# Kernel tuning notes

Measured on AMD Instinct MI355X. Metric: run time of the kernel, lower is better.

## Reference

```python
import jax, jax.numpy as jnp
import numpy as np

# FrictionConfig constants (chosen in init_kwargs)
K_STEPS = 4
ETA = 0.1
ETA_DECAY = 0.9
MU_MAX = 10.0
SMOOTH_LAMBDA = 0.1
RADIUS = 8
B, S, H = 4, 2048, 1024
INNER = max(H // 2, 32)  # 512


def _build_window_edges(length, radius):
    chunks = []
    for d in range(1, radius + 1):
        i = np.arange(length - d, dtype=np.int32)
        chunks.append(np.stack([i, i + d], axis=1))
    return np.concatenate(chunks, axis=0)  # [E, 2]


def setup_inputs() -> dict:
    key = jax.random.key(0)
    ks = jax.random.split(key, 8)
    hidden = jax.random.normal(ks[0], (B, S, H), dtype=jnp.float32)
    attention_mask = jnp.ones((B, S), dtype=jnp.int32)
    edges = jnp.asarray(_build_window_edges(S, RADIUS))
    # edge_mlp: Linear(2, INNER) -> GELU -> Linear(INNER, 1)
    W1 = jax.random.normal(ks[1], (2, INNER), dtype=jnp.float32) * (1.0 / np.sqrt(2))
    b1 = jnp.zeros((INNER,), dtype=jnp.float32)
    W2 = jax.random.normal(ks[2], (INNER, 1), dtype=jnp.float32) * (1.0 / np.sqrt(INNER))
    b2 = jnp.zeros((1,), dtype=jnp.float32)
    # q_proj: Linear(H, H)
    Wq = jax.random.normal(ks[3], (H, H), dtype=jnp.float32) * (1.0 / np.sqrt(H))
    bq = jnp.zeros((H,), dtype=jnp.float32)
    # LayerNorm
    gamma = jnp.ones((H,), dtype=jnp.float32)
    beta = jnp.zeros((H,), dtype=jnp.float32)
    return {"hidden": hidden, "attention_mask": attention_mask, "edges": edges,
            "Wq": Wq, "bq": bq, "W1": W1, "b1": b1, "W2": W2, "b2": b2,
            "gamma": gamma, "beta": beta}


def _edge_weights(h, ei, ej, W1, b1, W2, b2):
    hi = h[ei]  # [E, H]
    hj = h[ej]
    diff = hi - hj
    dist = jnp.linalg.norm(diff, axis=-1, keepdims=True)           # [E, 1]
    ni = jnp.maximum(jnp.linalg.norm(hi, axis=-1), 1e-6)
    nj = jnp.maximum(jnp.linalg.norm(hj, axis=-1), 1e-6)
    cos = (jnp.sum(hi * hj, axis=-1) / (ni * nj))[:, None]         # [E, 1]
    feats = jnp.concatenate([dist, cos], axis=-1)                  # [E, 2]
    z = jax.nn.gelu(feats @ W1 + b1, approximate=False) @ W2 + b2  # [E, 1]
    return jax.nn.softplus(z) + 1e-5


def _laplacian(h, ei, ej, mu):
    n = h.shape[0]
    weighted = mu * (h[ei] - h[ej])  # [E, H]
    # normalize_laplacian = True
    w = mu[:, 0]
    deg = jnp.zeros((n,), h.dtype).at[ei].add(w).at[ej].add(w)
    inv_sqrt = jnp.maximum(deg, 1e-6) ** -0.5
    weighted = weighted * (inv_sqrt[ei] * inv_sqrt[ej])[:, None]
    lap = jnp.zeros_like(h).at[ei].add(weighted).at[ej].add(-weighted)
    return lap


def _smooth(s):
    left = jnp.concatenate([s[:1], s[:-1]], axis=0)
    right = jnp.concatenate([s[1:], s[-1:]], axis=0)
    return s - SMOOTH_LAMBDA * (2.0 * s - left - right)


def _layernorm(x, gamma, beta):
    m = x.mean(axis=-1, keepdims=True)
    v = x.var(axis=-1, keepdims=True)
    return (x - m) * jax.lax.rsqrt(v + 1e-5) * gamma + beta


def _run_single(h, ei, ej, Wq, bq, W1, b1, W2, b2, gamma, beta):
    q = h @ Wq + bq
    state = h
    mu = None
    for step in range(K_STEPS):
        mu = _edge_weights(state, ei, ej, W1, b1, W2, b2)  # recompute_mu=True
        mu = jnp.minimum(mu, MU_MAX)
        lap = _laplacian(state, ei, ej, mu)
        eta = ETA * (ETA_DECAY ** step)
        state = state - eta * (lap - q)
        state = _smooth(state)
    out = _layernorm(state + h, gamma, beta)
    diffs = state[ei] - state[ej]
    energy = 0.5 * jnp.sum(mu[:, 0] * jnp.sum(diffs * diffs, axis=-1))
    return out, energy


def reference(hidden, attention_mask, edges, Wq, bq, W1, b1, W2, b2, gamma, beta):
    # All masks are full-length, so edges are identical across batch and
    # the outer Python batch loop vectorizes to a vmap.
    ei, ej = edges[:, 0], edges[:, 1]
    outputs, energy = jax.vmap(
        lambda h: _run_single(h, ei, ej, Wq, bq, W1, b1, W2, b2, gamma, beta)
    )(hidden)
    return outputs, energy
```

## Files before the change

### kernel.cpp

```cpp
#include <hip/hip_runtime.h>

#define BB 4
#define SS 2048
#define HH 1024
#define TG 8
#define TU 32
#define CW 256

typedef unsigned short u16;
typedef __bf16 bf16x8 __attribute__((ext_vector_type(8)));
typedef float f32x4 __attribute__((ext_vector_type(4)));

__device__ __forceinline__ float b2f(u16 u){
  union { unsigned int i; float f; } v; v.i = ((unsigned int)u) << 16; return v.f;
}
__device__ __forceinline__ u16 f2b(float f){
  union { float f; unsigned int i; } v; v.f = f;
  unsigned int x = v.i;
  return (u16)((x + 0x7fffu + ((x >> 16) & 1u)) >> 16);
}
__device__ __forceinline__ float4 u4f(ushort4 v){
  float4 o; o.x = b2f(v.x); o.y = b2f(v.y); o.z = b2f(v.z); o.w = b2f(v.w); return o;
}
__device__ __forceinline__ ushort4 f4u(float4 v){
  ushort4 o; o.x = f2b(v.x); o.y = f2b(v.y); o.z = f2b(v.z); o.w = f2b(v.w); return o;
}
__device__ __forceinline__ float wave_sum(float v){
  #pragma unroll
  for(int m = 32; m > 0; m >>= 1) v += __shfl_xor(v, m);
  return v;
}
__device__ __forceinline__ float pread(const void* p, int i, int f){
  return f ? b2f(((const u16*)p)[i]) : ((const float*)p)[i];
}
__device__ __forceinline__ void gload16(const void* g, void* l){
  __builtin_amdgcn_global_load_lds((const __attribute__((address_space(1))) unsigned int*)g,
                                   (__attribute__((address_space(3))) unsigned int*)l, 16, 0, 0);
}
__device__ __forceinline__ float fast_gelu(float z){
  float x  = z * 0.70710678118654752f;
  float ax = fabsf(x);
  float t  = __builtin_amdgcn_rcpf(fmaf(0.3275911f, ax, 1.f));
  float poly = ((((1.061405429f*t - 1.453152027f)*t + 1.421413741f)*t
                 - 0.284496736f)*t + 0.254829592f)*t;
  float er = fmaf(-poly, __expf(-ax*ax), 1.f);
  er = (x < 0.f) ? -er : er;
  return 0.5f*z*(1.f + er);
}

__global__ __launch_bounds__(256) void k_params(const void* bq, const void* W1, const void* b1,
                                                const void* W2, const void* b2, const void* gm,
                                                const void* bt, float* bqc, float* W1c, float* b1c,
                                                float* W2c, float* b2c, float* gmc, float* btc,
                                                int* flagp){
  __shared__ int sf;
  if(threadIdx.x == 0){
    int f = (((const u16*)gm)[0] == 0x3F80u) ? 1 : 0;
    sf = f; *flagp = f;
  }
  __syncthreads();
  int f = sf, t = threadIdx.x;
  for(int i = t; i < 1024; i += 256) bqc[i] = pread(bq, i, f);
  for(int i = t; i < 1024; i += 256) W1c[i] = pread(W1, i, f);
  for(int i = t; i <  512; i += 256) b1c[i] = pread(b1, i, f);
  for(int i = t; i <  512; i += 256) W2c[i] = pread(W2, i, f);
  if(t == 0) b2c[0] = pread(b2, 0, f);
  for(int i = t; i < 1024; i += 256) gmc[i] = pread(gm, i, f);
  for(int i = t; i < 1024; i += 256) btc[i] = pread(bt, i, f);
}

__global__ __launch_bounds__(256) void k_cvt(const void* h, u16* s, const int* flagp){
  int f = *flagp;
  size_t i4 = (size_t)blockIdx.x*256 + threadIdx.x;
  if(f){
    ((ushort4*)s)[i4] = ((const ushort4*)h)[i4];
  } else {
    float4 v = ((const float4*)h)[i4];
    ((ushort4*)s)[i4] = f4u(v);
  }
}

__global__ __launch_bounds__(256) void k_transpose(const void* W, u16* __restrict__ Wt,
                                                   const int* flagp){
  int f = *flagp;
  __shared__ u16 t[32][33];
  int bx = blockIdx.x, by = blockIdx.y;
  int tx = threadIdx.x, ty = threadIdx.y;
  #pragma unroll
  for(int r = 0; r < 32; r += 8){
    int idx = (by*32 + ty + r)*HH + bx*32 + tx;
    float v = f ? b2f(((const u16*)W)[idx]) : ((const float*)W)[idx];
    t[ty + r][tx] = f2b(v);
  }
  __syncthreads();
  #pragma unroll
  for(int r = 0; r < 32; r += 8)
    Wt[(size_t)(bx*32 + ty + r)*HH + by*32 + tx] = t[tx][ty + r];
}

__global__ __launch_bounds__(256) void k_qgemm(const u16* __restrict__ A, const u16* __restrict__ Wt,
                                               const float* __restrict__ bqc, u16* __restrict__ q){
  __shared__ u16 lA[128*32];
  __shared__ u16 lB[128*32];
  int m0 = blockIdx.x*128, n0 = blockIdx.y*128;
  int tid  = threadIdx.x;
  int wave = tid >> 6, lane = tid & 63;
  int wm = (wave >> 1)*64, wn = (wave & 1)*64;
  int quad = lane >> 4, l16 = lane & 15;
  int srow = tid >> 2;
  int scol = (tid & 3)*8;

  f32x4 acc[4][4];
  #pragma unroll
  for(int i = 0; i < 4; i++)
    #pragma unroll
    for(int j = 0; j < 4; j++) acc[i][j] = (f32x4){0.f,0.f,0.f,0.f};

  for(int k0 = 0; k0 < HH; k0 += 32){
    __syncthreads();
    gload16(A  + (size_t)(m0 + srow     )*HH + k0 + scol, &lA[ srow     *32 + scol]);
    gload16(A  + (size_t)(m0 + srow + 64)*HH + k0 + scol, &lA[(srow+64) *32 + scol]);
    gload16(Wt + (size_t)(n0 + srow     )*HH + k0 + scol, &lB[ srow     *32 + scol]);
    gload16(Wt + (size_t)(n0 + srow + 64)*HH + k0 + scol, &lB[(srow+64) *32 + scol]);
    __syncthreads();
    bf16x8 af[4];
    #pragma unroll
    for(int mt = 0; mt < 4; mt++)
      af[mt] = *(const bf16x8*)&lA[(wm + mt*16 + l16)*32 + quad*8];
    #pragma unroll
    for(int nt = 0; nt < 4; nt++){
      bf16x8 bf = *(const bf16x8*)&lB[(wn + nt*16 + l16)*32 + quad*8];
      #pragma unroll
      for(int mt = 0; mt < 4; mt++)
        acc[mt][nt] = __builtin_amdgcn_mfma_f32_16x16x32_bf16(af[mt], bf, acc[mt][nt], 0, 0, 0);
    }
  }
  #pragma unroll
  for(int nt = 0; nt < 4; nt++){
    int col = n0 + wn + nt*16 + l16;
    float bqv = bqc[col];
    #pragma unroll
    for(int mt = 0; mt < 4; mt++){
      #pragma unroll
      for(int r = 0; r < 4; r++){
        int row = m0 + wm + mt*16 + quad*4 + r;
        q[(size_t)row*HH + col] = f2b(acc[mt][nt][r] + bqv);
      }
    }
  }
}

__global__ __launch_bounds__(128) void k_gram_mu(const u16* __restrict__ s,
                                                 const float* __restrict__ W1c, const float* __restrict__ b1c,
                                                 const float* __restrict__ W2c, const float* __restrict__ b2c,
                                                 float* __restrict__ mu){
  __shared__ float Gband[16*9];
  __shared__ float4 wpk[512];
  int b = blockIdx.y, i0 = blockIdx.x*TG;
  int tid = threadIdx.x, wave = tid >> 6, lane = tid & 63;

  #pragma unroll
  for(int i = tid; i < 512; i += 128)
    wpk[i] = make_float4(W1c[i], W1c[512+i], b1c[i], W2c[i]);

  if(wave == 0){
    int quad = lane >> 4, l16 = lane & 15;
    int ra = i0 + l16; if(ra > SS-1) ra = SS-1;
    const u16* ar = s + ((size_t)b*SS + ra)*HH + quad*8;
    f32x4 acc = (f32x4){0.f,0.f,0.f,0.f};
    #pragma unroll 8
    for(int k0 = 0; k0 < HH; k0 += 32){
      bf16x8 af = *(const bf16x8*)(ar + k0);
      acc = __builtin_amdgcn_mfma_f32_16x16x32_bf16(af, af, acc, 0, 0, 0);
    }
    #pragma unroll
    for(int r = 0; r < 4; r++){
      int gr = quad*4 + r;
      int dd = l16 - gr;
      if(dd >= 0 && dd <= 8) Gband[gr*9 + dd] = acc[r];
    }
  }
  __syncthreads();

  int e = tid >> 1, h = tid & 1;
  int d = (e >> 3) + 1, k = e & 7;
  bool valid = (i0 + k + d) < SS;
  float gii = Gband[k*9], gjj = Gband[(k+d)*9], gij = Gband[k*9 + d];
  float dist = sqrtf(fmaxf(gii + gjj - 2.f*gij, 0.f));
  float ni = fmaxf(sqrtf(gii), 1e-6f);
  float nj = fmaxf(sqrtf(gjj), 1e-6f);
  float cosv = gij * __builtin_amdgcn_rcpf(ni * nj);
  float acc = 0.f;
  const float4* wp = &wpk[h*256];
  #pragma unroll 4
  for(int j0 = 0; j0 < 256; j0++){
    float4 wv = wp[j0];
    float z1 = fmaf(dist, wv.x, fmaf(cosv, wv.y, wv.z));
    acc = fmaf(fast_gelu(z1), wv.w, acc);
  }
  acc += __shfl_xor(acc, 1);
  if(h == 0 && valid){
    float z  = acc + b2c[0];
    float sp = fmaxf(z, 0.f) + __logf(1.f + __expf(-fabsf(z)));
    mu[((size_t)b*8 + (d-1))*SS + (i0 + k)] = fminf(sp + 1e-5f, 10.0f);
  }
}

__global__ __launch_bounds__(256) void k_upsm(const u16* __restrict__ sIn, u16* __restrict__ sOut,
                                              const u16* __restrict__ q, const float* __restrict__ mu,
                                              float eta){
  __shared__ u16 st[50*CW];
  __shared__ u16 up[34*CW];
  __shared__ float invsS[50];
  __shared__ float muS[58*8];
  int i0 = blockIdx.x*TU, c0 = blockIdx.y*CW, b = blockIdx.z;
  int tid = threadIdx.x;

  for(int idx = tid; idx < 58*8; idx += 256){
    int ir = idx >> 3, d = (idx & 7) + 1;
    int i = i0 - 17 + ir;
    float v = 0.f;
    if(i >= 0 && i + d < SS) v = mu[((size_t)b*8 + d-1)*SS + i];
    muS[idx] = v;
  }
  for(int idx = tid; idx < 50*(CW/4); idx += 256){
    int r = idx / (CW/4), cc = idx % (CW/4);
    int i = i0 - 9 + r;
    ushort4 v = {0,0,0,0};
    if(i >= 0 && i < SS) v = *(const ushort4*)(sIn + ((size_t)b*SS + i)*HH + c0 + cc*4);
    ((ushort4*)st)[idx] = v;
  }
  __syncthreads();
  if(tid < 50){
    int ir = tid + 8;
    float deg = 0.f;
    #pragma unroll
    for(int d = 1; d <= 8; d++){
      deg += muS[ir*8 + d-1];
      deg += muS[(ir-d)*8 + d-1];
    }
    invsS[tid] = 1.0f / sqrtf(fmaxf(deg, 1e-6f));
  }
  __syncthreads();

  int rq = tid >> 6, lane = tid & 63;
  for(int jr = 0; jr < 9; jr++){
    int r = rq + jr*4;
    if(r >= 34) break;
    int i = i0 - 1 + r;
    if(i < 0 || i >= SS) continue;
    int sr = r + 8, vr = r + 8, mr = r + 16;
    float inv_i = invsS[vr];
    float4 si = u4f(((const ushort4*)(st + (size_t)sr*CW))[lane]);
    float A = 0.f;
    float4 acc = {0.f,0.f,0.f,0.f};
    #pragma unroll
    for(int d = 1; d <= 8; d++){
      float cR = muS[mr*8 + d-1]     * inv_i        * invsS[vr+d];
      float cL = muS[(mr-d)*8 + d-1] * invsS[vr-d]  * inv_i;
      A += cR + cL;
      float4 vR = u4f(((const ushort4*)(st + (size_t)(sr+d)*CW))[lane]);
      float4 vL = u4f(((const ushort4*)(st + (size_t)(sr-d)*CW))[lane]);
      acc.x -= cR*vR.x + cL*vL.x; acc.y -= cR*vR.y + cL*vL.y;
      acc.z -= cR*vR.z + cL*vL.z; acc.w -= cR*vR.w + cL*vL.w;
    }
    acc.x += A*si.x; acc.y += A*si.y; acc.z += A*si.z; acc.w += A*si.w;
    float4 qv = u4f(*(const ushort4*)(q + ((size_t)b*SS + i)*HH + c0 + lane*4));
    float4 o;
    o.x = si.x - eta*(acc.x - qv.x);
    o.y = si.y - eta*(acc.y - qv.y);
    o.z = si.z - eta*(acc.z - qv.z);
    o.w = si.w - eta*(acc.w - qv.w);
    ((ushort4*)(up + (size_t)r*CW))[lane] = f4u(o);
  }
  __syncthreads();
  for(int js = 0; js < 8; js++){
    int rr = rq + js*4;
    int i = i0 + rr;
    int ur = rr + 1;
    float4 c  = u4f(((const ushort4*)(up + (size_t)ur*CW))[lane]);
    float4 l  = (i > 0)      ? u4f(((const ushort4*)(up + (size_t)(ur-1)*CW))[lane]) : c;
    float4 r4 = (i < SS-1)   ? u4f(((const ushort4*)(up + (size_t)(ur+1)*CW))[lane]) : c;
    float4 o;
    o.x = c.x - 0.1f*(2.f*c.x - l.x - r4.x);
    o.y = c.y - 0.1f*(2.f*c.y - l.y - r4.y);
    o.z = c.z - 0.1f*(2.f*c.z - l.z - r4.z);
    o.w = c.w - 0.1f*(2.f*c.w - l.w - r4.w);
    *(ushort4*)(sOut + ((size_t)b*SS + i)*HH + c0 + lane*4) = f4u(o);
  }
}

__global__ __launch_bounds__(256) void k_out(const u16* __restrict__ sA, const void* __restrict__ hraw,
                                             const float* __restrict__ gmc, const float* __restrict__ btc,
                                             void* __restrict__ outp, const int* flagp){
  int f = *flagp;
  int b = blockIdx.x >> 11, i = blockIdx.x & (SS-1);
  int tid = threadIdx.x;
  size_t row = (size_t)b*SS + i;
  float4 sv = u4f(((const ushort4*)(sA + row*HH))[tid]);
  float4 hv;
  if(f) hv = u4f(((const ushort4*)((const u16*)hraw + row*HH))[tid]);
  else  hv = ((const float4*)((const float*)hraw + row*HH))[tid];
  float x0 = sv.x + hv.x, x1 = sv.y + hv.y, x2 = sv.z + hv.z, x3 = sv.w + hv.w;

  __shared__ float sh[4];
  int wv = tid >> 6, lane = tid & 63;
  float lsum = wave_sum(x0 + x1 + x2 + x3);
  if(lane == 0) sh[wv] = lsum;
  __syncthreads();
  float mean = (sh[0] + sh[1] + sh[2] + sh[3]) * (1.f/HH);
  __syncthreads();
  float d0 = x0-mean, d1 = x1-mean, d2 = x2-mean, d3 = x3-mean;
  float lsq = wave_sum(d0*d0 + d1*d1 + d2*d2 + d3*d3);
  if(lane == 0) sh[wv] = lsq;
  __syncthreads();
  float var = (sh[0] + sh[1] + sh[2] + sh[3]) * (1.f/HH);
  float sc = 1.0f / sqrtf(var + 1e-5f);

  int col = tid*4;
  float4 o;
  o.x = d0*sc*gmc[col+0] + btc[col+0];
  o.y = d1*sc*gmc[col+1] + btc[col+1];
  o.z = d2*sc*gmc[col+2] + btc[col+2];
  o.w = d3*sc*gmc[col+3] + btc[col+3];
  if(f) ((ushort4*)((u16*)outp + row*HH))[tid] = f4u(o);
  else  ((float4*)((float*)outp + row*HH))[tid] = o;
}

__global__ __launch_bounds__(128) void k_energy(const u16* __restrict__ s, const float* __restrict__ mu,
                                                float* __restrict__ partials){
  __shared__ float Gband[16*9];
  int b = blockIdx.y, i0 = blockIdx.x*TG;
  int tid = threadIdx.x, wave = tid >> 6, lane = tid & 63;

  if(wave == 0){
    int quad = lane >> 4, l16 = lane & 15;
    int ra = i0 + l16; if(ra > SS-1) ra = SS-1;
    const u16* ar = s + ((size_t)b*SS + ra)*HH + quad*8;
    f32x4 acc = (f32x4){0.f,0.f,0.f,0.f};
    #pragma unroll 8
    for(int k0 = 0; k0 < HH; k0 += 32){
      bf16x8 af = *(const bf16x8*)(ar + k0);
      acc = __builtin_amdgcn_mfma_f32_16x16x32_bf16(af, af, acc, 0, 0, 0);
    }
    #pragma unroll
    for(int r = 0; r < 4; r++){
      int gr = quad*4 + r;
      int dd = l16 - gr;
      if(dd >= 0 && dd <= 8) Gband[gr*9 + dd] = acc[r];
    }
  }
  __syncthreads();
  if(wave == 0){
    int d = (lane >> 3) + 1, k = lane & 7;
    float esum = 0.f;
    if((i0 + k + d) < SS){
      float d2 = fmaxf(Gband[k*9] + Gband[(k+d)*9] - 2.f*Gband[k*9 + d], 0.f);
      esum = mu[((size_t)b*8 + (d-1))*SS + (i0 + k)] * d2;
    }
    esum = wave_sum(esum);
    if(lane == 0) partials[(size_t)b*256 + blockIdx.x] = esum;
  }
}

__global__ __launch_bounds__(256) void k_efinal(const float* __restrict__ partials, void* __restrict__ outp,
                                                const int* flagp){
  int f = *flagp;
  int b = blockIdx.x;
  float sacc = partials[(size_t)b*256 + threadIdx.x];
  sacc = wave_sum(sacc);
  __shared__ float sh[4];
  if((threadIdx.x & 63) == 0) sh[threadIdx.x >> 6] = sacc;
  __syncthreads();
  if(threadIdx.x == 0){
    float e = 0.5f * (sh[0] + sh[1] + sh[2] + sh[3]);
    if(f) ((u16*)outp)[(size_t)BB*SS*HH + b] = f2b(e);
    else  ((float*)outp)[(size_t)BB*SS*HH + b] = e;
  }
}

extern "C" void kernel_launch(void* const* d_in, const int* in_sizes, int n_in,
                              void* d_out, int out_size, void* d_ws, size_t ws_size,
                              hipStream_t stream) {
  const void* hidden = d_in[0];
  const void* Wq  = d_in[3];
  const void* bq  = d_in[4];
  const void* W1  = d_in[5];
  const void* b1  = d_in[6];
  const void* W2  = d_in[7];
  const void* b2v = d_in[8];
  const void* gamma = d_in[9];
  const void* beta  = d_in[10];

  char* w = (char*)d_ws;
  u16*   q   = (u16*)w;   w += (size_t)BB*SS*HH*2;
  u16*   sA  = (u16*)w;   w += (size_t)BB*SS*HH*2;
  u16*   Wt  = (u16*)w;   w += (size_t)HH*HH*2;
  float* mu  = (float*)w; w += (size_t)BB*8*SS*4;
  float* partials = (float*)w; w += (size_t)BB*256*4;
  float* bqc = (float*)w; w += 1024*4;
  float* W1c = (float*)w; w += 1024*4;
  float* b1c = (float*)w; w += 512*4;
  float* W2c = (float*)w; w += 512*4;
  float* b2c = (float*)w; w += 4;
  float* gmc = (float*)w; w += 1024*4;
  float* btc = (float*)w; w += 1024*4;
  int*   flagp = (int*)w; w += 4;
  u16* sB = (u16*)d_out;

  k_params   <<<1, 256, 0, stream>>>(bq, W1, b1, W2, b2v, gamma, beta,
                                     bqc, W1c, b1c, W2c, b2c, gmc, btc, flagp);
  k_cvt      <<<(BB*SS*HH/4)/256, 256, 0, stream>>>(hidden, sA, flagp);
  k_transpose<<<dim3(HH/32, HH/32), dim3(32,8), 0, stream>>>(Wq, Wt, flagp);
  k_qgemm    <<<dim3(BB*SS/128, HH/128), 256, 0, stream>>>(sA, Wt, bqc, q);

  const float etas[4] = {0.1f, 0.09f, 0.081f, 0.0729f};
  for(int step = 0; step < 4; step++){
    const u16* cur = (step & 1) ? sB : sA;
    u16*       nxt = (step & 1) ? sA : sB;
    k_gram_mu<<<dim3(SS/TG, BB), 128, 0, stream>>>(cur, W1c, b1c, W2c, b2c, mu);
    k_upsm   <<<dim3(SS/TU, HH/CW, BB), 256, 0, stream>>>(cur, nxt, q, mu, etas[step]);
  }
  k_out   <<<BB*SS, 256, 0, stream>>>(sA, hidden, gmc, btc, d_out, flagp);
  k_energy<<<dim3(SS/TG, BB), 128, 0, stream>>>(sA, mu, partials);
  k_efinal<<<BB, 256, 0, stream>>>(partials, d_out, flagp);
}
```

Baseline: 415.8 us.

## Fuse all stages into one persistent megakernel with grid-wide barriers

Replaces the sequence of separate launches (param convert, cast, transpose, q GEMM, per-step gram/mu and update/smooth kernels, layernorm, energy) with a single persistent kernel that loops over work units and uses a software grid barrier between phases. The gram computation is also split across all four waves with partial Gram reductions in shared memory, and the MLP loop is split four ways per edge. This is meant to remove launch overhead and idle tails between the many small kernels. In exchange it relies on all blocks being co-resident (grid sized from occupancy queries), adds atomic spin-barrier cost, and may lose per-kernel tuning such as occupancy for the GEMM phase.

Result: slower. 977.9 us (+135.2%).

```diff
diff --git a/kernel.cpp b/kernel.cpp
--- a/kernel.cpp
+++ b/kernel.cpp
@@ -3,13 +3,32 @@
 #define BB 4
 #define SS 2048
 #define HH 1024
-#define TG 8
 #define TU 32
 #define CW 256
+#define MAXG 768
 
 typedef unsigned short u16;
 typedef __bf16 bf16x8 __attribute__((ext_vector_type(8)));
 typedef float f32x4 __attribute__((ext_vector_type(4)));
+
+#define SMEM_BYTES 45072
+#define OFF_ST    0
+#define OFF_UP    25600
+#define OFF_MUS   43008
+#define OFF_INV   44864
+#define OFF_WPK   0
+#define OFF_GPART 8192
+#define OFF_GBAND 10496
+#define OFF_LA    0
+#define OFF_LB    8192
+
+#define QBYTES   ((size_t)BB*SS*HH*2)
+#define WS_Q     ((size_t)0)
+#define WS_SA    QBYTES
+#define WS_WT    (2*QBYTES)
+#define WS_MU    (2*QBYTES + (size_t)HH*HH*2)
+#define WS_PART  (WS_MU + (size_t)BB*8*SS*4)
+#define WS_PAR   (WS_PART + 4096)
 
 __device__ __forceinline__ float b2f(u16 u){
   union { unsigned int i; float f; } v; v.i = ((unsigned int)u) << 16; return v.f;
@@ -48,380 +67,390 @@
   return 0.5f*z*(1.f + er);
 }
 
-__global__ __launch_bounds__(256) void k_params(const void* bq, const void* W1, const void* b1,
-                                                const void* W2, const void* b2, const void* gm,
-                                                const void* bt, float* bqc, float* W1c, float* b1c,
-                                                float* W2c, float* b2c, float* gmc, float* btc,
-                                                int* flagp){
-  __shared__ int sf;
-  if(threadIdx.x == 0){
-    int f = (((const u16*)gm)[0] == 0x3F80u) ? 1 : 0;
-    sf = f; *flagp = f;
-  }
-  __syncthreads();
-  int f = sf, t = threadIdx.x;
-  for(int i = t; i < 1024; i += 256) bqc[i] = pread(bq, i, f);
-  for(int i = t; i < 1024; i += 256) W1c[i] = pread(W1, i, f);
-  for(int i = t; i <  512; i += 256) b1c[i] = pread(b1, i, f);
-  for(int i = t; i <  512; i += 256) W2c[i] = pread(W2, i, f);
-  if(t == 0) b2c[0] = pread(b2, 0, f);
-  for(int i = t; i < 1024; i += 256) gmc[i] = pread(gm, i, f);
-  for(int i = t; i < 1024; i += 256) btc[i] = pread(bt, i, f);
-}
-
-__global__ __launch_bounds__(256) void k_cvt(const void* h, u16* s, const int* flagp){
-  int f = *flagp;
-  size_t i4 = (size_t)blockIdx.x*256 + threadIdx.x;
-  if(f){
-    ((ushort4*)s)[i4] = ((const ushort4*)h)[i4];
-  } else {
-    float4 v = ((const float4*)h)[i4];
-    ((ushort4*)s)[i4] = f4u(v);
-  }
-}
-
-__global__ __launch_bounds__(256) void k_transpose(const void* W, u16* __restrict__ Wt,
-                                                   const int* flagp){
-  int f = *flagp;
-  __shared__ u16 t[32][33];
-  int bx = blockIdx.x, by = blockIdx.y;
-  int tx = threadIdx.x, ty = threadIdx.y;
-  #pragma unroll
-  for(int r = 0; r < 32; r += 8){
-    int idx = (by*32 + ty + r)*HH + bx*32 + tx;
-    float v = f ? b2f(((const u16*)W)[idx]) : ((const float*)W)[idx];
-    t[ty + r][tx] = f2b(v);
-  }
-  __syncthreads();
-  #pragma unroll
-  for(int r = 0; r < 32; r += 8)
-    Wt[(size_t)(bx*32 + ty + r)*HH + by*32 + tx] = t[tx][ty + r];
-}
-
-__global__ __launch_bounds__(256) void k_qgemm(const u16* __restrict__ A, const u16* __restrict__ Wt,
-                                               const float* __restrict__ bqc, u16* __restrict__ q){
-  __shared__ u16 lA[128*32];
-  __shared__ u16 lB[128*32];
-  int m0 = blockIdx.x*128, n0 = blockIdx.y*128;
-  int tid  = threadIdx.x;
-  int wave = tid >> 6, lane = tid & 63;
-  int wm = (wave >> 1)*64, wn = (wave & 1)*64;
-  int quad = lane >> 4, l16 = lane & 15;
-  int srow = tid >> 2;
-  int scol = (tid & 3)*8;
-
-  f32x4 acc[4][4];
-  #pragma unroll
-  for(int i = 0; i < 4; i++)
-    #pragma unroll
-    for(int j = 0; j < 4; j++) acc[i][j] = (f32x4){0.f,0.f,0.f,0.f};
-
-  for(int k0 = 0; k0 < HH; k0 += 32){
-    __syncthreads();
-    gload16(A  + (size_t)(m0 + srow     )*HH + k0 + scol, &lA[ srow     *32 + scol]);
-    gload16(A  + (size_t)(m0 + srow + 64)*HH + k0 + scol, &lA[(srow+64) *32 + scol]);
-    gload16(Wt + (size_t)(n0 + srow     )*HH + k0 + scol, &lB[ srow     *32 + scol]);
-    gload16(Wt + (size_t)(n0 + srow + 64)*HH + k0 + scol, &lB[(srow+64) *32 + scol]);
-    __syncthreads();
-    bf16x8 af[4];
-    #pragma unroll
-    for(int mt = 0; mt < 4; mt++)
-      af[mt] = *(const bf16x8*)&lA[(wm + mt*16 + l16)*32 + quad*8];
-    #pragma unroll
-    for(int nt = 0; nt < 4; nt++){
-      bf16x8 bf = *(const bf16x8*)&lB[(wn + nt*16 + l16)*32 + quad*8];
-      #pragma unroll
-      for(int mt = 0; mt < 4; mt++)
-        acc[mt][nt] = __builtin_amdgcn_mfma_f32_16x16x32_bf16(af[mt], bf, acc[mt][nt], 0, 0, 0);
-    }
-  }
-  #pragma unroll
-  for(int nt = 0; nt < 4; nt++){
-    int col = n0 + wn + nt*16 + l16;
-    float bqv = bqc[col];
-    #pragma unroll
-    for(int mt = 0; mt < 4; mt++){
-      #pragma unroll
-      for(int r = 0; r < 4; r++){
-        int row = m0 + wm + mt*16 + quad*4 + r;
-        q[(size_t)row*HH + col] = f2b(acc[mt][nt][r] + bqv);
-      }
-    }
-  }
-}
-
-__global__ __launch_bounds__(128) void k_gram_mu(const u16* __restrict__ s,
-                                                 const float* __restrict__ W1c, const float* __restrict__ b1c,
-                                                 const float* __restrict__ W2c, const float* __restrict__ b2c,
-                                                 float* __restrict__ mu){
-  __shared__ float Gband[16*9];
-  __shared__ float4 wpk[512];
-  int b = blockIdx.y, i0 = blockIdx.x*TG;
-  int tid = threadIdx.x, wave = tid >> 6, lane = tid & 63;
-
-  #pragma unroll
-  for(int i = tid; i < 512; i += 128)
-    wpk[i] = make_float4(W1c[i], W1c[512+i], b1c[i], W2c[i]);
-
-  if(wave == 0){
-    int quad = lane >> 4, l16 = lane & 15;
-    int ra = i0 + l16; if(ra > SS-1) ra = SS-1;
-    const u16* ar = s + ((size_t)b*SS + ra)*HH + quad*8;
-    f32x4 acc = (f32x4){0.f,0.f,0.f,0.f};
-    #pragma unroll 8
-    for(int k0 = 0; k0 < HH; k0 += 32){
-      bf16x8 af = *(const bf16x8*)(ar + k0);
-      acc = __builtin_amdgcn_mfma_f32_16x16x32_bf16(af, af, acc, 0, 0, 0);
-    }
-    #pragma unroll
-    for(int r = 0; r < 4; r++){
-      int gr = quad*4 + r;
-      int dd = l16 - gr;
-      if(dd >= 0 && dd <= 8) Gband[gr*9 + dd] = acc[r];
-    }
-  }
-  __syncthreads();
-
-  int e = tid >> 1, h = tid & 1;
-  int d = (e >> 3) + 1, k = e & 7;
-  bool valid = (i0 + k + d) < SS;
-  float gii = Gband[k*9], gjj = Gband[(k+d)*9], gij = Gband[k*9 + d];
-  float dist = sqrtf(fmaxf(gii + gjj - 2.f*gij, 0.f));
-  float ni = fmaxf(sqrtf(gii), 1e-6f);
-  float nj = fmaxf(sqrtf(gjj), 1e-6f);
-  float cosv = gij * __builtin_amdgcn_rcpf(ni * nj);
-  float acc = 0.f;
-  const float4* wp = &wpk[h*256];
-  #pragma unroll 4
-  for(int j0 = 0; j0 < 256; j0++){
-    float4 wv = wp[j0];
-    float z1 = fmaf(dist, wv.x, fmaf(cosv, wv.y, wv.z));
-    acc = fmaf(fast_gelu(z1), wv.w, acc);
-  }
-  acc += __shfl_xor(acc, 1);
-  if(h == 0 && valid){
-    float z  = acc + b2c[0];
-    float sp = fmaxf(z, 0.f) + __logf(1.f + __expf(-fabsf(z)));
-    mu[((size_t)b*8 + (d-1))*SS + (i0 + k)] = fminf(sp + 1e-5f, 10.0f);
-  }
-}
-
-__global__ __launch_bounds__(256) void k_upsm(const u16* __restrict__ sIn, u16* __restrict__ sOut,
-                                              const u16* __restrict__ q, const float* __restrict__ mu,
-                                              float eta){
-  __shared__ u16 st[50*CW];
-  __shared__ u16 up[34*CW];
-  __shared__ float invsS[50];
-  __shared__ float muS[58*8];
-  int i0 = blockIdx.x*TU, c0 = blockIdx.y*CW, b = blockIdx.z;
-  int tid = threadIdx.x;
-
-  for(int idx = tid; idx < 58*8; idx += 256){
-    int ir = idx >> 3, d = (idx & 7) + 1;
-    int i = i0 - 17 + ir;
-    float v = 0.f;
-    if(i >= 0 && i + d < SS) v = mu[((size_t)b*8 + d-1)*SS + i];
-    muS[idx] = v;
-  }
-  for(int idx = tid; idx < 50*(CW/4); idx += 256){
-    int r = idx / (CW/4), cc = idx % (CW/4);
-    int i = i0 - 9 + r;
-    ushort4 v = {0,0,0,0};
-    if(i >= 0 && i < SS) v = *(const ushort4*)(sIn + ((size_t)b*SS + i)*HH + c0 + cc*4);
-    ((ushort4*)st)[idx] = v;
-  }
-  __syncthreads();
-  if(tid < 50){
-    int ir = tid + 8;
-    float deg = 0.f;
-    #pragma unroll
-    for(int d = 1; d <= 8; d++){
-      deg += muS[ir*8 + d-1];
-      deg += muS[(ir-d)*8 + d-1];
-    }
-    invsS[tid] = 1.0f / sqrtf(fmaxf(deg, 1e-6f));
-  }
-  __syncthreads();
-
-  int rq = tid >> 6, lane = tid & 63;
-  for(int jr = 0; jr < 9; jr++){
-    int r = rq + jr*4;
-    if(r >= 34) break;
-    int i = i0 - 1 + r;
-    if(i < 0 || i >= SS) continue;
-    int sr = r + 8, vr = r + 8, mr = r + 16;
-    float inv_i = invsS[vr];
-    float4 si = u4f(((const ushort4*)(st + (size_t)sr*CW))[lane]);
-    float A = 0.f;
-    float4 acc = {0.f,0.f,0.f,0.f};
-    #pragma unroll
-    for(int d = 1; d <= 8; d++){
-      float cR = muS[mr*8 + d-1]     * inv_i        * invsS[vr+d];
-      float cL = muS[(mr-d)*8 + d-1] * invsS[vr-d]  * inv_i;
-      A += cR + cL;
-      float4 vR = u4f(((const ushort4*)(st + (size_t)(sr+d)*CW))[lane]);
-      float4 vL = u4f(((const ushort4*)(st + (size_t)(sr-d)*CW))[lane]);
-      acc.x -= cR*vR.x + cL*vL.x; acc.y -= cR*vR.y + cL*vL.y;
-      acc.z -= cR*vR.z + cL*vL.z; acc.w -= cR*vR.w + cL*vL.w;
-    }
-    acc.x += A*si.x; acc.y += A*si.y; acc.z += A*si.z; acc.w += A*si.w;
-    float4 qv = u4f(*(const ushort4*)(q + ((size_t)b*SS + i)*HH + c0 + lane*4));
-    float4 o;
-    o.x = si.x - eta*(acc.x - qv.x);
-    o.y = si.y - eta*(acc.y - qv.y);
-    o.z = si.z - eta*(acc.z - qv.z);
-    o.w = si.w - eta*(acc.w - qv.w);
-    ((ushort4*)(up + (size_t)r*CW))[lane] = f4u(o);
-  }
-  __syncthreads();
-  for(int js = 0; js < 8; js++){
-    int rr = rq + js*4;
-    int i = i0 + rr;
-    int ur = rr + 1;
-    float4 c  = u4f(((const ushort4*)(up + (size_t)ur*CW))[lane]);
-    float4 l  = (i > 0)      ? u4f(((const ushort4*)(up + (size_t)(ur-1)*CW))[lane]) : c;
-    float4 r4 = (i < SS-1)   ? u4f(((const ushort4*)(up + (size_t)(ur+1)*CW))[lane]) : c;
-    float4 o;
-    o.x = c.x - 0.1f*(2.f*c.x - l.x - r4.x);
-    o.y = c.y - 0.1f*(2.f*c.y - l.y - r4.y);
-    o.z = c.z - 0.1f*(2.f*c.z - l.z - r4.z);
-    o.w = c.w - 0.1f*(2.f*c.w - l.w - r4.w);
-    *(ushort4*)(sOut + ((size_t)b*SS + i)*HH + c0 + lane*4) = f4u(o);
-  }
-}
-
-__global__ __launch_bounds__(256) void k_out(const u16* __restrict__ sA, const void* __restrict__ hraw,
-                                             const float* __restrict__ gmc, const float* __restrict__ btc,
-                                             void* __restrict__ outp, const int* flagp){
-  int f = *flagp;
-  int b = blockIdx.x >> 11, i = blockIdx.x & (SS-1);
-  int tid = threadIdx.x;
-  size_t row = (size_t)b*SS + i;
-  float4 sv = u4f(((const ushort4*)(sA + row*HH))[tid]);
-  float4 hv;
-  if(f) hv = u4f(((const ushort4*)((const u16*)hraw + row*HH))[tid]);
-  else  hv = ((const float4*)((const float*)hraw + row*HH))[tid];
-  float x0 = sv.x + hv.x, x1 = sv.y + hv.y, x2 = sv.z + hv.z, x3 = sv.w + hv.w;
-
-  __shared__ float sh[4];
-  int wv = tid >> 6, lane = tid & 63;
-  float lsum = wave_sum(x0 + x1 + x2 + x3);
-  if(lane == 0) sh[wv] = lsum;
-  __syncthreads();
-  float mean = (sh[0] + sh[1] + sh[2] + sh[3]) * (1.f/HH);
-  __syncthreads();
-  float d0 = x0-mean, d1 = x1-mean, d2 = x2-mean, d3 = x3-mean;
-  float lsq = wave_sum(d0*d0 + d1*d1 + d2*d2 + d3*d3);
-  if(lane == 0) sh[wv] = lsq;
-  __syncthreads();
-  float var = (sh[0] + sh[1] + sh[2] + sh[3]) * (1.f/HH);
-  float sc = 1.0f / sqrtf(var + 1e-5f);
-
-  int col = tid*4;
-  float4 o;
-  o.x = d0*sc*gmc[col+0] + btc[col+0];
-  o.y = d1*sc*gmc[col+1] + btc[col+1];
-  o.z = d2*sc*gmc[col+2] + btc[col+2];
-  o.w = d3*sc*gmc[col+3] + btc[col+3];
-  if(f) ((ushort4*)((u16*)outp + row*HH))[tid] = f4u(o);
-  else  ((float4*)((float*)outp + row*HH))[tid] = o;
-}
-
-__global__ __launch_bounds__(128) void k_energy(const u16* __restrict__ s, const float* __restrict__ mu,
-                                                float* __restrict__ partials){
-  __shared__ float Gband[16*9];
-  int b = blockIdx.y, i0 = blockIdx.x*TG;
-  int tid = threadIdx.x, wave = tid >> 6, lane = tid & 63;
-
-  if(wave == 0){
-    int quad = lane >> 4, l16 = lane & 15;
-    int ra = i0 + l16; if(ra > SS-1) ra = SS-1;
-    const u16* ar = s + ((size_t)b*SS + ra)*HH + quad*8;
-    f32x4 acc = (f32x4){0.f,0.f,0.f,0.f};
-    #pragma unroll 8
-    for(int k0 = 0; k0 < HH; k0 += 32){
-      bf16x8 af = *(const bf16x8*)(ar + k0);
-      acc = __builtin_amdgcn_mfma_f32_16x16x32_bf16(af, af, acc, 0, 0, 0);
-    }
-    #pragma unroll
-    for(int r = 0; r < 4; r++){
-      int gr = quad*4 + r;
-      int dd = l16 - gr;
-      if(dd >= 0 && dd <= 8) Gband[gr*9 + dd] = acc[r];
-    }
-  }
-  __syncthreads();
-  if(wave == 0){
-    int d = (lane >> 3) + 1, k = lane & 7;
-    float esum = 0.f;
-    if((i0 + k + d) < SS){
-      float d2 = fmaxf(Gband[k*9] + Gband[(k+d)*9] - 2.f*Gband[k*9 + d], 0.f);
-      esum = mu[((size_t)b*8 + (d-1))*SS + (i0 + k)] * d2;
-    }
-    esum = wave_sum(esum);
-    if(lane == 0) partials[(size_t)b*256 + blockIdx.x] = esum;
-  }
-}
-
-__global__ __launch_bounds__(256) void k_efinal(const float* __restrict__ partials, void* __restrict__ outp,
-                                                const int* flagp){
-  int f = *flagp;
-  int b = blockIdx.x;
-  float sacc = partials[(size_t)b*256 + threadIdx.x];
-  sacc = wave_sum(sacc);
-  __shared__ float sh[4];
-  if((threadIdx.x & 63) == 0) sh[threadIdx.x >> 6] = sacc;
+__device__ __forceinline__ void grid_sync(unsigned int* bar, int nb){
   __syncthreads();
   if(threadIdx.x == 0){
-    float e = 0.5f * (sh[0] + sh[1] + sh[2] + sh[3]);
-    if(f) ((u16*)outp)[(size_t)BB*SS*HH + b] = f2b(e);
-    else  ((float*)outp)[(size_t)BB*SS*HH + b] = e;
-  }
-}
-
-extern "C" void kernel_launch(void* const* d_in, const int* in_sizes, int n_in,
-                              void* d_out, int out_size, void* d_ws, size_t ws_size,
-                              hipStream_t stream) {
-  const void* hidden = d_in[0];
-  const void* Wq  = d_in[3];
-  const void* bq  = d_in[4];
-  const void* W1  = d_in[5];
-  const void* b1  = d_in[6];
-  const void* W2  = d_in[7];
-  const void* b2v = d_in[8];
-  const void* gamma = d_in[9];
-  const void* beta  = d_in[10];
-
-  char* w = (char*)d_ws;
-  u16*   q   = (u16*)w;   w += (size_t)BB*SS*HH*2;
-  u16*   sA  = (u16*)w;   w += (size_t)BB*SS*HH*2;
-  u16*   Wt  = (u16*)w;   w += (size_t)HH*HH*2;
-  float* mu  = (float*)w; w += (size_t)BB*8*SS*4;
-  float* partials = (float*)w; w += (size_t)BB*256*4;
-  float* bqc = (float*)w; w += 1024*4;
-  float* W1c = (float*)w; w += 1024*4;
-  float* b1c = (float*)w; w += 512*4;
-  float* W2c = (float*)w; w += 512*4;
-  float* b2c = (float*)w; w += 4;
-  float* gmc = (float*)w; w += 1024*4;
-  float* btc = (float*)w; w += 1024*4;
-  int*   flagp = (int*)w; w += 4;
-  u16* sB = (u16*)d_out;
-
-  k_params   <<<1, 256, 0, stream>>>(bq, W1, b1, W2, b2v, gamma, beta,
-                                     bqc, W1c, b1c, W2c, b2c, gmc, btc, flagp);
-  k_cvt      <<<(BB*SS*HH/4)/256, 256, 0, stream>>>(hidden, sA, flagp);
-  k_transpose<<<dim3(HH/32, HH/32), dim3(32,8), 0, stream>>>(Wq, Wt, flagp);
-  k_qgemm    <<<dim3(BB*SS/128, HH/128), 256, 0, stream>>>(sA, Wt, bqc, q);
+    __threadfence();
+    unsigned int gen = __hip_atomic_load(&bar[1], __ATOMIC_RELAXED, __HIP_MEMORY_SCOPE_AGENT);
+    unsigned int n = __hip_atomic_fetch_add(&bar[0], 1u, __ATOMIC_ACQ_REL, __HIP_MEMORY_SCOPE_AGENT);
+    if(n == (unsigned int)nb - 1u){
+      __hip_atomic_store(&bar[0], 0u, __ATOMIC_RELAXED, __HIP_MEMORY_SCOPE_AGENT);
+      __hip_atomic_store(&bar[1], gen + 1u, __ATOMIC_RELEASE, __HIP_MEMORY_SCOPE_AGENT);
+    } else {
+      while(__hip_atomic_load(&bar[1], __ATOMIC_ACQUIRE, __HIP_MEMORY_SCOPE_AGENT) == gen)
+        __builtin_amdgcn_s_sleep(2);
+    }
+    __threadfence();
+  }
+  __syncthreads();
+}
+
+__global__ void k_init0(unsigned int* bar){ bar[threadIdx.x] = 0u; }
+
+__global__ __launch_bounds__(256, 3) void k_mega(
+    const void* __restrict__ hidden, const void* __restrict__ Wq,
+    const void* __restrict__ bq, const void* __restrict__ W1,
+    const void* __restrict__ b1v, const void* __restrict__ W2,
+    const void* __restrict__ b2v, const void* __restrict__ gm,
+    const void* __restrict__ bt, void* __restrict__ outp,
+    char* __restrict__ ws, int nb)
+{
+  __shared__ __align__(16) char smem[SMEM_BYTES];
+  u16*   q    = (u16*)(ws + WS_Q);
+  u16*   sA   = (u16*)(ws + WS_SA);
+  u16*   Wt   = (u16*)(ws + WS_WT);
+  float* mu   = (float*)(ws + WS_MU);
+  float* part = (float*)(ws + WS_PART);
+  float* bqc  = (float*)(ws + WS_PAR + 0);
+  float* W1c  = (float*)(ws + WS_PAR + 4096);
+  float* b1c  = (float*)(ws + WS_PAR + 8192);
+  float* W2c  = (float*)(ws + WS_PAR + 10240);
+  float* b2c  = (float*)(ws + WS_PAR + 12288);
+  float* gmc  = (float*)(ws + WS_PAR + 12304);
+  float* btc  = (float*)(ws + WS_PAR + 16400);
+  int*   flagp= (int*)(ws + WS_PAR + 20496);
+  unsigned int* bar = (unsigned int*)(ws + WS_PAR + 20512);
+  u16* sB = (u16*)outp;
+
+  int tid = threadIdx.x, bid = blockIdx.x;
+  int wave = tid >> 6, lane = tid & 63;
+
+  if(bid == 0){
+    int f0 = (((const u16*)gm)[0] == 0x3F80u) ? 1 : 0;
+    if(tid == 0) *flagp = f0;
+    for(int i = tid; i < 1024; i += 256) bqc[i] = pread(bq, i, f0);
+    for(int i = tid; i < 1024; i += 256) W1c[i] = pread(W1, i, f0);
+    for(int i = tid; i <  512; i += 256) b1c[i] = pread(b1v, i, f0);
+    for(int i = tid; i <  512; i += 256) W2c[i] = pread(W2, i, f0);
+    if(tid == 0) b2c[0] = pread(b2v, 0, f0);
+    for(int i = tid; i < 1024; i += 256) gmc[i] = pread(gm, i, f0);
+    for(int i = tid; i < 1024; i += 256) btc[i] = pread(bt, i, f0);
+  }
+  grid_sync(bar, nb);
+  int f = *flagp;
+
+  for(size_t i4 = (size_t)bid*256 + tid; i4 < (size_t)BB*SS*HH/4; i4 += (size_t)nb*256){
+    if(f) ((ushort4*)sA)[i4] = ((const ushort4*)hidden)[i4];
+    else  ((ushort4*)sA)[i4] = f4u(((const float4*)hidden)[i4]);
+  }
+  {
+    u16 (*tsh)[33] = (u16(*)[33])smem;
+    int tx = tid & 31, ty = tid >> 5;
+    for(int t = bid; t < 1024; t += nb){
+      int bx = t & 31, by = t >> 5;
+      __syncthreads();
+      #pragma unroll
+      for(int r = 0; r < 32; r += 8){
+        int idx = (by*32 + ty + r)*HH + bx*32 + tx;
+        float v = f ? b2f(((const u16*)Wq)[idx]) : ((const float*)Wq)[idx];
+        tsh[ty + r][tx] = f2b(v);
+      }
+      __syncthreads();
+      #pragma unroll
+      for(int r = 0; r < 32; r += 8)
+        Wt[(size_t)(bx*32 + ty + r)*HH + by*32 + tx] = tsh[tx][ty + r];
+    }
+  }
+  grid_sync(bar, nb);
+
+  {
+    u16* lA = (u16*)(smem + OFF_LA);
+    u16* lB = (u16*)(smem + OFF_LB);
+    int wm = (wave >> 1)*64, wn = (wave & 1)*64;
+    int quad = lane >> 4, l16 = lane & 15;
+    int srow = tid >> 2, scol = (tid & 3)*8;
+    for(int u = bid; u < 512; u += nb){
+      int m0 = (u & 63)*128, n0 = (u >> 6)*128;
+      f32x4 acc[4][4];
+      #pragma unroll
+      for(int i = 0; i < 4; i++)
+        #pragma unroll
+        for(int j = 0; j < 4; j++) acc[i][j] = (f32x4){0.f,0.f,0.f,0.f};
+      for(int k0 = 0; k0 < HH; k0 += 32){
+        __syncthreads();
+        gload16(sA + (size_t)(m0 + srow     )*HH + k0 + scol, &lA[ srow     *32 + scol]);
+        gload16(sA + (size_t)(m0 + srow + 64)*HH + k0 + scol, &lA[(srow+64) *32 + scol]);
+        gload16(Wt + (size_t)(n0 + srow     )*HH + k0 + scol, &lB[ srow     *32 + scol]);
+        gload16(Wt + (size_t)(n0 + srow + 64)*HH + k0 + scol, &lB[(srow+64) *32 + scol]);
+        __syncthreads();
+        bf16x8 af[4];
+        #pragma unroll
+        for(int mt = 0; mt < 4; mt++)
+          af[mt] = *(const bf16x8*)&lA[(wm + mt*16 + l16)*32 + quad*8];
+        #pragma unroll
+        for(int nt = 0; nt < 4; nt++){
+          bf16x8 bf = *(const bf16x8*)&lB[(wn + nt*16 + l16)*32 + quad*8];
+          #pragma unroll
+          for(int mt = 0; mt < 4; mt++)
+            acc[mt][nt] = __builtin_amdgcn_mfma_f32_16x16x32_bf16(af[mt], bf, acc[mt][nt], 0, 0, 0);
+        }
+      }
+      #pragma unroll
+      for(int nt = 0; nt < 4; nt++){
+        int col = n0 + wn + nt*16 + l16;
+        float bqv = bqc[col];
+        #pragma unroll
+        for(int mt = 0; mt < 4; mt++){
+          #pragma unroll
+          for(int r = 0; r < 4; r++){
+            int row = m0 + wm + mt*16 + quad*4 + r;
+            q[(size_t)row*HH + col] = f2b(acc[mt][nt][r] + bqv);
+          }
+        }
+      }
+      __syncthreads();
+    }
+  }
+  grid_sync(bar, nb);
 
   const float etas[4] = {0.1f, 0.09f, 0.081f, 0.0729f};
   for(int step = 0; step < 4; step++){
     const u16* cur = (step & 1) ? sB : sA;
     u16*       nxt = (step & 1) ? sA : sB;
-    k_gram_mu<<<dim3(SS/TG, BB), 128, 0, stream>>>(cur, W1c, b1c, W2c, b2c, mu);
-    k_upsm   <<<dim3(SS/TU, HH/CW, BB), 256, 0, stream>>>(cur, nxt, q, mu, etas[step]);
-  }
-  k_out   <<<BB*SS, 256, 0, stream>>>(sA, hidden, gmc, btc, d_out, flagp);
-  k_energy<<<dim3(SS/TG, BB), 128, 0, stream>>>(sA, mu, partials);
-  k_efinal<<<BB, 256, 0, stream>>>(partials, d_out, flagp);
-}
+
+    {
+      float4* wpk  = (float4*)(smem + OFF_WPK);
+      float* Gpart = (float*)(smem + OFF_GPART);
+      float* Gband = (float*)(smem + OFF_GBAND);
+      __syncthreads();
+      for(int i = tid; i < 512; i += 256)
+        wpk[i] = make_float4(W1c[i], W1c[512+i], b1c[i], W2c[i]);
+      float b2cv = b2c[0];
+      int quad = lane >> 4, l16 = lane & 15;
+      for(int u = bid; u < 1024; u += nb){
+        int b = u >> 8, i0 = (u & 255)*8;
+        for(int i2 = lane; i2 < 144; i2 += 64) Gpart[wave*144 + i2] = 0.f;
+        __syncthreads();
+        {
+          int ra = i0 + l16; if(ra > SS-1) ra = SS-1;
+          const u16* ar = cur + ((size_t)b*SS + ra)*HH + wave*256 + quad*8;
+          f32x4 acc = (f32x4){0.f,0.f,0.f,0.f};
+          #pragma unroll
+          for(int k0 = 0; k0 < 256; k0 += 32){
+            bf16x8 af = *(const bf16x8*)(ar + k0);
+            acc = __builtin_amdgcn_mfma_f32_16x16x32_bf16(af, af, acc, 0, 0, 0);
+          }
+          #pragma unroll
+          for(int r = 0; r < 4; r++){
+            int gr = quad*4 + r, dd = l16 - gr;
+            if(dd >= 0 && dd <= 8) Gpart[wave*144 + gr*9 + dd] = acc[r];
+          }
+        }
+        __syncthreads();
+        if(tid < 144) Gband[tid] = Gpart[tid] + Gpart[144+tid] + Gpart[288+tid] + Gpart[432+tid];
+        __syncthreads();
+        {
+          int e = tid >> 2, qh = tid & 3;
+          int d = (e >> 3) + 1, k = e & 7;
+          bool valid = (i0 + k + d) < SS;
+          float gii = Gband[k*9], gjj = Gband[(k+d)*9], gij = Gband[k*9 + d];
+          float dist = sqrtf(fmaxf(gii + gjj - 2.f*gij, 0.f));
+          float ni = fmaxf(sqrtf(gii), 1e-6f);
+          float nj = fmaxf(sqrtf(gjj), 1e-6f);
+          float cosv = gij * __builtin_amdgcn_rcpf(ni * nj);
+          float acc = 0.f;
+          const float4* wp = &wpk[qh*128];
+          #pragma unroll 4
+          for(int j0 = 0; j0 < 128; j0++){
+            float4 wv = wp[j0];
+            float z1 = fmaf(dist, wv.x, fmaf(cosv, wv.y, wv.z));
+            acc = fmaf(fast_gelu(z1), wv.w, acc);
+          }
+          acc += __shfl_xor(acc, 1);
+          acc += __shfl_xor(acc, 2);
+          if(qh == 0 && valid){
+            float z  = acc + b2cv;
+            float sp = fmaxf(z, 0.f) + __logf(1.f + __expf(-fabsf(z)));
+            mu[((size_t)b*8 + (d-1))*SS + (i0 + k)] = fminf(sp + 1e-5f, 10.0f);
+          }
+        }
+        __syncthreads();
+      }
+    }
+    grid_sync(bar, nb);
+
+    {
+      u16*  st    = (u16*)(smem + OFF_ST);
+      u16*  up    = (u16*)(smem + OFF_UP);
+      float* muS  = (float*)(smem + OFF_MUS);
+      float* invsS= (float*)(smem + OFF_INV);
+      float eta = etas[step];
+      __syncthreads();
+      for(int u = bid; u < 1024; u += nb){
+        int b = u >> 8, rem = u & 255;
+        int i0 = (rem >> 2)*TU, c0 = (rem & 3)*CW;
+        for(int idx = tid; idx < 58*8; idx += 256){
+          int ir = idx >> 3, d = (idx & 7) + 1;
+          int i = i0 - 17 + ir;
+          float v = 0.f;
+          if(i >= 0 && i + d < SS) v = mu[((size_t)b*8 + d-1)*SS + i];
+          muS[idx] = v;
+        }
+        for(int idx = tid; idx < 50*(CW/4); idx += 256){
+          int r = idx / (CW/4), cc = idx % (CW/4);
+          int i = i0 - 9 + r;
+          ushort4 v = {0,0,0,0};
+          if(i >= 0 && i < SS) v = *(const ushort4*)(cur + ((size_t)b*SS + i)*HH + c0 + cc*4);
+          ((ushort4*)st)[idx] = v;
+        }
+        __syncthreads();
+        if(tid < 50){
+          int ir = tid + 8;
+          float deg = 0.f;
+          #pragma unroll
+          for(int d = 1; d <= 8; d++){
+            deg += muS[ir*8 + d-1];
+            deg += muS[(ir-d)*8 + d-1];
+          }
+          invsS[tid] = 1.0f / sqrtf(fmaxf(deg, 1e-6f));
+        }
+        __syncthreads();
+        for(int jr = 0; jr < 9; jr++){
+          int r = wave + jr*4;
+          if(r >= 34) break;
+          int i = i0 - 1 + r;
+          if(i < 0 || i >= SS) continue;
+          int sr = r + 8, vr = r + 8, mr = r + 16;
+          float inv_i = invsS[vr];
+          float4 si = u4f(((const ushort4*)(st + (size_t)sr*CW))[lane]);
+          float A = 0.f;
+          float4 acc = {0.f,0.f,0.f,0.f};
+          #pragma unroll
+          for(int d = 1; d <= 8; d++){
+            float cR = muS[mr*8 + d-1]     * inv_i       * invsS[vr+d];
+            float cL = muS[(mr-d)*8 + d-1] * invsS[vr-d] * inv_i;
+            A += cR + cL;
+            float4 vR = u4f(((const ushort4*)(st + (size_t)(sr+d)*CW))[lane]);
+            float4 vL = u4f(((const ushort4*)(st + (size_t)(sr-d)*CW))[lane]);
+            acc.x -= cR*vR.x + cL*vL.x; acc.y -= cR*vR.y + cL*vL.y;
+            acc.z -= cR*vR.z + cL*vL.z; acc.w -= cR*vR.w + cL*vL.w;
+          }
+          acc.x += A*si.x; acc.y += A*si.y; acc.z += A*si.z; acc.w += A*si.w;
+          float4 qv = u4f(*(const ushort4*)(q + ((size_t)b*SS + i)*HH + c0 + lane*4));
+          float4 o;
+          o.x = si.x - eta*(acc.x - qv.x);
+          o.y = si.y - eta*(acc.y - qv.y);
+          o.z = si.z - eta*(acc.z - qv.z);
+          o.w = si.w - eta*(acc.w - qv.w);
+          ((ushort4*)(up + (size_t)r*CW))[lane] = f4u(o);
+        }
+        __syncthreads();
+        for(int js = 0; js < 8; js++){
+          int rr = wave + js*4;
+          int i = i0 + rr;
+          int ur = rr + 1;
+          float4 c  = u4f(((const ushort4*)(up + (size_t)ur*CW))[lane]);
+          float4 l  = (i > 0)    ? u4f(((const ushort4*)(up + (size_t)(ur-1)*CW))[lane]) : c;
+          float4 r4 = (i < SS-1) ? u4f(((const ushort4*)(up + (size_t)(ur+1)*CW))[lane]) : c;
+          float4 o;
+          o.x = c.x - 0.1f*(2.f*c.x - l.x - r4.x);
+          o.y = c.y - 0.1f*(2.f*c.y - l.y - r4.y);
+          o.z = c.z - 0.1f*(2.f*c.z - l.z - r4.z);
+          o.w = c.w - 0.1f*(2.f*c.w - l.w - r4.w);
+          *(ushort4*)(nxt + ((size_t)b*SS + i)*HH + c0 + lane*4) = f4u(o);
+        }
+        __syncthreads();
+      }
+    }
+    grid_sync(bar, nb);
+  }
+
+  {
+    float* shred = (float*)smem;
+    __syncthreads();
+    for(int r = bid; r < BB*SS; r += nb){
+      size_t row = (size_t)r;
+      float4 sv = u4f(((const ushort4*)(sA + row*HH))[tid]);
+      float4 hv;
+      if(f) hv = u4f(((const ushort4*)((const u16*)hidden + row*HH))[tid]);
+      else  hv = ((const float4*)((const float*)hidden + row*HH))[tid];
+      float x0 = sv.x + hv.x, x1 = sv.y + hv.y, x2 = sv.z + hv.z, x3 = sv.w + hv.w;
+      float lsum = wave_sum(x0 + x1 + x2 + x3);
+      if(lane == 0) shred[wave] = lsum;
+      __syncthreads();
+      float mean = (shred[0] + shred[1] + shred[2] + shred[3]) * (1.f/HH);
+      __syncthreads();
+      float d0 = x0-mean, d1 = x1-mean, d2 = x2-mean, d3 = x3-mean;
+      float lsq = wave_sum(d0*d0 + d1*d1 + d2*d2 + d3*d3);
+      if(lane == 0) shred[wave] = lsq;
+      __syncthreads();
+      float var = (shred[0] + shred[1] + shred[2] + shred[3]) * (1.f/HH);
+      float sc = 1.0f / sqrtf(var + 1e-5f);
+      int col = tid*4;
+      float4 o;
+      o.x = d0*sc*gmc[col+0] + btc[col+0];
+      o.y = d1*sc*gmc[col+1] + btc[col+1];
+      o.z = d2*sc*gmc[col+2] + btc[col+2];
+      o.w = d3*sc*gmc[col+3] + btc[col+3];
+      if(f) ((ushort4*)((u16*)outp + row*HH))[tid] = f4u(o);
+      else  ((float4*)((float*)outp + row*HH))[tid] = o;
+      __syncthreads();
+    }
+    float* Gpart = (float*)(smem + OFF_GPART);
+    float* Gband = (float*)(smem + OFF_GBAND);
+    int quad = lane >> 4, l16 = lane & 15;
+    for(int u = bid; u < 1024; u += nb){
+      int b = u >> 8, i0 = (u & 255)*8;
+      for(int i2 = lane; i2 < 144; i2 += 64) Gpart[wave*144 + i2] = 0.f;
+      __syncthreads();
+      {
+        int ra = i0 + l16; if(ra > SS-1) ra = SS-1;
+        const u16* ar = sA + ((size_t)b*SS + ra)*HH + wave*256 + quad*8;
+        f32x4 acc = (f32x4){0.f,0.f,0.f,0.f};
+        #pragma unroll
+        for(int k0 = 0; k0 < 256; k0 += 32){
+          bf16x8 af = *(const bf16x8*)(ar + k0);
+          acc = __builtin_amdgcn_mfma_f32_16x16x32_bf16(af, af, acc, 0, 0, 0);
+        }
+        #pragma unroll
+        for(int r = 0; r < 4; r++){
+          int gr = quad*4 + r, dd = l16 - gr;
+          if(dd >= 0 && dd <= 8) Gpart[wave*144 + gr*9 + dd] = acc[r];
+        }
+      }
+      __syncthreads();
+      if(tid < 144) Gband[tid] = Gpart[tid] + Gpart[144+tid] + Gpart[288+tid] + Gpart[432+tid];
+      __syncthreads();
+      if(tid < 64){
+        int d = (tid >> 3) + 1, k = tid & 7;
+        float esum = 0.f;
+        if((i0 + k + d) < SS){
+          float d2 = fmaxf(Gband[k*9] + Gband[(k+d)*9] - 2.f*Gband[k*9 + d], 0.f);
+          esum = mu[((size_t)b*8 + (d-1))*SS + (i0 + k)] * d2;
+        }
+        esum = wave_sum(esum);
+        if(tid == 0) part[u] = esum;
+      }
+      __syncthreads();
+    }
+  }
+  grid_sync(bar, nb);
+
+  if(bid == 0){
+    float v = part[wave*256 + lane]       + part[wave*256 + 64 + lane]
+            + part[wave*256 + 128 + lane] + part[wave*256 + 192 + lane];
+    v = wave_sum(v);
+    if(lane == 0){
+      float en = 0.5f * v;
+      if(f) ((u16*)outp)[(size_t)BB*SS*HH + wave] = f2b(en);
+      else  ((float*)outp)[(size_t)BB*SS*HH + wave] = en;
+    }
+  }
+}
+
+extern "C" void kernel_launch(void* const* d_in, const int* in_sizes, int n_in,
+                              void* d_out, int out_size, void* d_ws, size_t ws_size,
+                              hipStream_t stream) {
+  char* ws = (char*)d_ws;
+  unsigned int* bar = (unsigned int*)(ws + WS_PAR + 20512);
+
+  int bpc = 0;
+  hipError_t e = hipOccupancyMaxActiveBlocksPerMultiprocessor(&bpc, k_mega, 256, 0);
+  int nb = (e == hipSuccess && bpc >= 1) ? bpc*256 : 512;
+  if(nb > MAXG) nb = MAXG;
+
+  k_init0<<<1, 2, 0, stream>>>(bar);
+  k_mega <<<nb, 256, 0, stream>>>(d_in[0], d_in[3], d_in[4], d_in[5], d_in[6],
+                                  d_in[7], d_in[8], d_in[9], d_in[10],
+                                  d_out, ws, nb);
+}
```
